# Performance work log

Measured on AMD Instinct MI355X. Metric: run time of the kernel, lower is better.

The kernel has to match this reference:

```python
import jax, jax.numpy as jnp
import numpy as np

B, D_IN, D_OUT = 131072, 256, 256

def setup_inputs() -> dict:
    key = jax.random.key(0)
    k1, k2, k3 = jax.random.split(key, 3)
    x = jax.random.normal(k1, (B, D_IN), dtype=jnp.float32)
    # One weight row / bias scalar per SingleNeuron, concatenated: [D_OUT, D_IN], [D_OUT]
    bound = 1.0 / np.sqrt(D_IN)  # nn.Linear default init scale
    W = jax.random.uniform(k2, (D_OUT, D_IN), dtype=jnp.float32, minval=-bound, maxval=bound)
    b = jax.random.uniform(k3, (D_OUT,), dtype=jnp.float32, minval=-bound, maxval=bound)
    return {"x": x, "W": W, "b": b}

def reference(x, W, b):
    # Fused equivalent of looping per-neuron Linear(in,1), stack(dim=1), squeeze, relu
    return jax.nn.relu(jnp.einsum('bi,oi->bo', x, W) + b)
```

## Files before the change

### kernel.cpp

```cpp
#include <hip/hip_runtime.h>


typedef __attribute__((ext_vector_type(16))) float f32x16;
typedef __attribute__((ext_vector_type(8))) __bf16 bf16x8;

#define MFMA(a, b, c) \
    (c) = __builtin_amdgcn_mfma_f32_32x32x16_bf16((a), (b), (c), 0, 0, 0)

__device__ __forceinline__ void cvt8(const float4& A, const float4& B,
                                     bf16x8& hi, bf16x8& lo) {
    const float f[8] = {A.x, A.y, A.z, A.w, B.x, B.y, B.z, B.w};
#pragma unroll
    for (int j = 0; j < 8; ++j) {
        const unsigned int u = __builtin_bit_cast(unsigned int, f[j]);
        hi[j] = __builtin_bit_cast(__bf16, (unsigned short)(u >> 16));
        const float hf = __builtin_bit_cast(float, u & 0xffff0000u);
        const float lf = f[j] - hf;
        lo[j] = __builtin_bit_cast(__bf16,
                    (unsigned short)(__builtin_bit_cast(unsigned int, lf) >> 16));
    }
}

__device__ __forceinline__ void gload16(const float* g, float* l) {
    __builtin_amdgcn_global_load_lds(
        (const __attribute__((address_space(1))) void*)g,
        (__attribute__((address_space(3))) void*)l, 16, 0, 0);
}

__global__ __launch_bounds__(256)
void wprep_kernel(const float* __restrict__ W,
                  __bf16* __restrict__ whi, __bf16* __restrict__ wlo) {
    const int wv = (int)blockIdx.x * 4 + (threadIdx.x >> 6);
    const int l  = threadIdx.x & 63;
    const int t  = wv & 15;
    const int F  = wv >> 4;
    const int n  = F * 32 + (l & 31);
    const int k  = t * 16 + (l >> 5) * 8;
    const float4 A = *(const float4*)(W + n * 256 + k);
    const float4 B = *(const float4*)(W + n * 256 + k + 4);
    bf16x8 hi, lo;
    cvt8(A, B, hi, lo);
    *(bf16x8*)(whi + wv * 512 + l * 8) = hi;
    *(bf16x8*)(wlo + wv * 512 + l * 8) = lo;
}

__global__ __launch_bounds__(512, 3)
void gemm_mfma_kernel(const float* __restrict__ x,
                      const __bf16* __restrict__ whi,
                      const __bf16* __restrict__ wlo,
                      const float* __restrict__ bias,
                      float* __restrict__ out) {
    __shared__ float xs[3][4096];

    const int tid  = threadIdx.x;
    const int lane = tid & 63;
    const int wid  = tid >> 6;
    const int wm   = wid >> 2;
    const int wn   = wid & 3;

    const int bid = (int)blockIdx.x;
    const int rt  = (bid & 7) * 128 + (bid >> 3);

    const int r31 = lane & 31;
    const int g   = lane >> 5;
    const long row0 = (long)rt * 128;

    const int m0 = wm * 64 + r31;
    const int m1 = m0 + 32;
    const int sw = r31 & 7;

    f32x16 acc[2][2];
#pragma unroll
    for (int i = 0; i < 2; ++i)
#pragma unroll
        for (int j = 0; j < 2; ++j)
#pragma unroll
            for (int r = 0; r < 16; ++r) acc[i][j][r] = 0.f;

    const int fbase0 = (wn * 2) * 16;
    const __bf16* whip = whi + (long)lane * 8;
    const __bf16* wlop = wlo + (long)lane * 8;

    auto STAGE = [&](int b, int chunk) {
#pragma unroll
        for (int j = 0; j < 2; ++j) {
            const int G = j * 512 + tid;
            const int m = G >> 3;
            const int cs = (G & 7) ^ (m & 7);
            const float* gp = x + (row0 + m) * 256 + chunk * 32 + cs * 4;
            float* lp = &xs[b][(j * 512 + wid * 64) * 4];
            gload16(gp, lp);
        }
    };

    auto TSTEP = [&](const float* xb, int t,
                     const bf16x8& bh0, const bf16x8& bl0,
                     const bf16x8& bh1, const bf16x8& bl1) {
        const int c0 = t * 4 + g * 2;
        const float4 A0a = *(const float4*)(xb + m0 * 32 + ((c0 ^ sw) * 4));
        const float4 A0b = *(const float4*)(xb + m0 * 32 + (((c0 + 1) ^ sw) * 4));
        const float4 A1a = *(const float4*)(xb + m1 * 32 + ((c0 ^ sw) * 4));
        const float4 A1b = *(const float4*)(xb + m1 * 32 + (((c0 + 1) ^ sw) * 4));
        bf16x8 ah0, al0, ah1, al1;
        cvt8(A0a, A0b, ah0, al0);
        cvt8(A1a, A1b, ah1, al1);
        MFMA(ah0, bh0, acc[0][0]); MFMA(ah0, bh1, acc[0][1]);
        MFMA(ah1, bh0, acc[1][0]); MFMA(ah1, bh1, acc[1][1]);
        MFMA(ah0, bl0, acc[0][0]); MFMA(ah0, bl1, acc[0][1]);
        MFMA(ah1, bl0, acc[1][0]); MFMA(ah1, bl1, acc[1][1]);
        MFMA(al0, bh0, acc[0][0]); MFMA(al0, bh1, acc[0][1]);
        MFMA(al1, bh0, acc[1][0]); MFMA(al1, bh1, acc[1][1]);
    };

#define CHUNK(c, VM)                                                          \
    {                                                                         \
        asm volatile("s_waitcnt vmcnt(" VM ")" ::: "memory");                 \
        __builtin_amdgcn_s_barrier();                                         \
        const long f0 = (long)(fbase0 + (c) * 2) * 512;                       \
        const long f1 = f0 + 16 * 512;                                        \
        const long h0 = (long)(fbase0 + (c) * 2 + 1) * 512;                   \
        const long h1 = h0 + 16 * 512;                                        \
        const bf16x8 B0h0 = *(const bf16x8*)(whip + f0);                      \
        const bf16x8 B0l0 = *(const bf16x8*)(wlop + f0);                      \
        const bf16x8 B0h1 = *(const bf16x8*)(whip + f1);                      \
        const bf16x8 B0l1 = *(const bf16x8*)(wlop + f1);                      \
        const bf16x8 B1h0 = *(const bf16x8*)(whip + h0);                      \
        const bf16x8 B1l0 = *(const bf16x8*)(wlop + h0);                      \
        const bf16x8 B1h1 = *(const bf16x8*)(whip + h1);                      \
        const bf16x8 B1l1 = *(const bf16x8*)(wlop + h1);                      \
        __builtin_amdgcn_sched_barrier(0);                                    \
        if ((c) + 2 < 8) STAGE(((c) + 2) % 3, (c) + 2);                       \
        const float* xb = &xs[(c) % 3][0];                                    \
        TSTEP(xb, 0, B0h0, B0l0, B0h1, B0l1);                                 \
        TSTEP(xb, 1, B1h0, B1l0, B1h1, B1l1);                                 \
    }

    STAGE(0, 0);
    STAGE(1, 1);
    CHUNK(0, "2")
    CHUNK(1, "2")
    CHUNK(2, "2")
    CHUNK(3, "2")
    CHUNK(4, "2")
    CHUNK(5, "2")
    CHUNK(6, "2")
    CHUNK(7, "0")
#undef CHUNK

    const int  ocol0 = wn * 64;
    const long orow0 = row0 + wm * 64;
    const float bj0 = bias[ocol0 + r31];
    const float bj1 = bias[ocol0 + 32 + r31];

#pragma unroll
    for (int i = 0; i < 2; ++i) {
#pragma unroll
        for (int r = 0; r < 16; ++r) {
            const int rowf = (r & 3) + 8 * (r >> 2) + 4 * g;
            const long row = orow0 + i * 32 + rowf;
            float v0 = acc[i][0][r] + bj0;
            float v1 = acc[i][1][r] + bj1;
            v0 = v0 > 0.f ? v0 : 0.f;
            v1 = v1 > 0.f ? v1 : 0.f;
            out[row * 256 + ocol0 + r31]      = v0;
            out[row * 256 + ocol0 + 32 + r31] = v1;
        }
    }
}

extern "C" void kernel_launch(void* const* d_in, const int* in_sizes, int n_in,
                              void* d_out, int out_size, void* d_ws, size_t ws_size,
                              hipStream_t stream) {
    (void)n_in; (void)ws_size; (void)out_size;
    const float* x = (const float*)d_in[0];
    const float* W = (const float*)d_in[1];
    const float* b = (const float*)d_in[2];
    float* out = (float*)d_out;

    __bf16* whi = (__bf16*)d_ws;
    __bf16* wlo = whi + 65536;

    wprep_kernel<<<32, 256, 0, stream>>>(W, whi, wlo);

    const int M = in_sizes[0] / 256;
    const int grid = M / 128;
    gemm_mfma_kernel<<<grid, 512, 0, stream>>>(x, whi, wlo, b, out);
}
```

Baseline: 263.6 us.

## Halve row tile to 64 per block and raise occupancy to four blocks

```diff
diff --git a/kernel.cpp b/kernel.cpp
--- a/kernel.cpp
+++ b/kernel.cpp
@@ -44,13 +44,13 @@
     *(bf16x8*)(wlo + wv * 512 + l * 8) = lo;
 }
 
-__global__ __launch_bounds__(512, 3)
+__global__ __launch_bounds__(512, 4)
 void gemm_mfma_kernel(const float* __restrict__ x,
                       const __bf16* __restrict__ whi,
                       const __bf16* __restrict__ wlo,
                       const float* __restrict__ bias,
                       float* __restrict__ out) {
-    __shared__ float xs[3][4096];
+    __shared__ float xs[3][2048];
 
     const int tid  = threadIdx.x;
     const int lane = tid & 63;
@@ -59,112 +59,88 @@
     const int wn   = wid & 3;
 
     const int bid = (int)blockIdx.x;
-    const int rt  = (bid & 7) * 128 + (bid >> 3);
+    const int rt  = (bid & 7) * 256 + (bid >> 3);
 
     const int r31 = lane & 31;
     const int g   = lane >> 5;
-    const long row0 = (long)rt * 128;
+    const long row0 = (long)rt * 64;
 
-    const int m0 = wm * 64 + r31;
-    const int m1 = m0 + 32;
+    const int m0 = wm * 32 + r31;
     const int sw = r31 & 7;
 
-    f32x16 acc[2][2];
+    f32x16 acc0, acc1;
 #pragma unroll
-    for (int i = 0; i < 2; ++i)
-#pragma unroll
-        for (int j = 0; j < 2; ++j)
-#pragma unroll
-            for (int r = 0; r < 16; ++r) acc[i][j][r] = 0.f;
+    for (int r = 0; r < 16; ++r) { acc0[r] = 0.f; acc1[r] = 0.f; }
 
     const int fbase0 = (wn * 2) * 16;
     const __bf16* whip = whi + (long)lane * 8;
     const __bf16* wlop = wlo + (long)lane * 8;
 
     auto STAGE = [&](int b, int chunk) {
-#pragma unroll
-        for (int j = 0; j < 2; ++j) {
-            const int G = j * 512 + tid;
-            const int m = G >> 3;
-            const int cs = (G & 7) ^ (m & 7);
-            const float* gp = x + (row0 + m) * 256 + chunk * 32 + cs * 4;
-            float* lp = &xs[b][(j * 512 + wid * 64) * 4];
-            gload16(gp, lp);
-        }
+        const int m = tid >> 3;
+        const int cs = (tid & 7) ^ (m & 7);
+        const float* gp = x + (row0 + m) * 256 + chunk * 32 + cs * 4;
+        float* lp = &xs[b][(wid * 64) * 4];
+        gload16(gp, lp);
     };
 
-    auto TSTEP = [&](const float* xb, int t,
-                     const bf16x8& bh0, const bf16x8& bl0,
-                     const bf16x8& bh1, const bf16x8& bl1) {
+    auto TSTEP = [&](const float* xb, int ks, int t) {
         const int c0 = t * 4 + g * 2;
-        const float4 A0a = *(const float4*)(xb + m0 * 32 + ((c0 ^ sw) * 4));
-        const float4 A0b = *(const float4*)(xb + m0 * 32 + (((c0 + 1) ^ sw) * 4));
-        const float4 A1a = *(const float4*)(xb + m1 * 32 + ((c0 ^ sw) * 4));
-        const float4 A1b = *(const float4*)(xb + m1 * 32 + (((c0 + 1) ^ sw) * 4));
-        bf16x8 ah0, al0, ah1, al1;
-        cvt8(A0a, A0b, ah0, al0);
-        cvt8(A1a, A1b, ah1, al1);
-        MFMA(ah0, bh0, acc[0][0]); MFMA(ah0, bh1, acc[0][1]);
-        MFMA(ah1, bh0, acc[1][0]); MFMA(ah1, bh1, acc[1][1]);
-        MFMA(ah0, bl0, acc[0][0]); MFMA(ah0, bl1, acc[0][1]);
-        MFMA(ah1, bl0, acc[1][0]); MFMA(ah1, bl1, acc[1][1]);
-        MFMA(al0, bh0, acc[0][0]); MFMA(al0, bh1, acc[0][1]);
-        MFMA(al1, bh0, acc[1][0]); MFMA(al1, bh1, acc[1][1]);
+        const float4 Aa = *(const float4*)(xb + m0 * 32 + ((c0 ^ sw) * 4));
+        const float4 Ab = *(const float4*)(xb + m0 * 32 + (((c0 + 1) ^ sw) * 4));
+        bf16x8 ah, al;
+        cvt8(Aa, Ab, ah, al);
+        const long f0 = (long)(fbase0 + ks) * 512;
+        const long f1 = f0 + 16 * 512;
+        {
+            const bf16x8 bh = *(const bf16x8*)(whip + f0);
+            const bf16x8 bl = *(const bf16x8*)(wlop + f0);
+            MFMA(ah, bh, acc0); MFMA(ah, bl, acc0); MFMA(al, bh, acc0);
+        }
+        {
+            const bf16x8 bh = *(const bf16x8*)(whip + f1);
+            const bf16x8 bl = *(const bf16x8*)(wlop + f1);
+            MFMA(ah, bh, acc1); MFMA(ah, bl, acc1); MFMA(al, bh, acc1);
+        }
     };
 
 #define CHUNK(c, VM)                                                          \
     {                                                                         \
         asm volatile("s_waitcnt vmcnt(" VM ")" ::: "memory");                 \
         __builtin_amdgcn_s_barrier();                                         \
-        const long f0 = (long)(fbase0 + (c) * 2) * 512;                       \
-        const long f1 = f0 + 16 * 512;                                        \
-        const long h0 = (long)(fbase0 + (c) * 2 + 1) * 512;                   \
-        const long h1 = h0 + 16 * 512;                                        \
-        const bf16x8 B0h0 = *(const bf16x8*)(whip + f0);                      \
-        const bf16x8 B0l0 = *(const bf16x8*)(wlop + f0);                      \
-        const bf16x8 B0h1 = *(const bf16x8*)(whip + f1);                      \
-        const bf16x8 B0l1 = *(const bf16x8*)(wlop + f1);                      \
-        const bf16x8 B1h0 = *(const bf16x8*)(whip + h0);                      \
-        const bf16x8 B1l0 = *(const bf16x8*)(wlop + h0);                      \
-        const bf16x8 B1h1 = *(const bf16x8*)(whip + h1);                      \
-        const bf16x8 B1l1 = *(const bf16x8*)(wlop + h1);                      \
-        __builtin_amdgcn_sched_barrier(0);                                    \
         if ((c) + 2 < 8) STAGE(((c) + 2) % 3, (c) + 2);                       \
         const float* xb = &xs[(c) % 3][0];                                    \
-        TSTEP(xb, 0, B0h0, B0l0, B0h1, B0l1);                                 \
-        TSTEP(xb, 1, B1h0, B1l0, B1h1, B1l1);                                 \
+        TSTEP(xb, (c) * 2, 0);                                                \
+        TSTEP(xb, (c) * 2 + 1, 1);                                            \
     }
 
     STAGE(0, 0);
     STAGE(1, 1);
-    CHUNK(0, "2")
-    CHUNK(1, "2")
-    CHUNK(2, "2")
-    CHUNK(3, "2")
-    CHUNK(4, "2")
-    CHUNK(5, "2")
-    CHUNK(6, "2")
+    CHUNK(0, "1")
+    CHUNK(1, "1")
+    CHUNK(2, "1")
+    CHUNK(3, "1")
+    CHUNK(4, "1")
+    CHUNK(5, "1")
+    CHUNK(6, "1")
     CHUNK(7, "0")
 #undef CHUNK
 
     const int  ocol0 = wn * 64;
-    const long orow0 = row0 + wm * 64;
+    const long orow0 = row0 + wm * 32;
     const float bj0 = bias[ocol0 + r31];
     const float bj1 = bias[ocol0 + 32 + r31];
 
 #pragma unroll
-    for (int i = 0; i < 2; ++i) {
-#pragma unroll
-        for (int r = 0; r < 16; ++r) {
-            const int rowf = (r & 3) + 8 * (r >> 2) + 4 * g;
-            const long row = orow0 + i * 32 + rowf;
-            float v0 = acc[i][0][r] + bj0;
-            float v1 = acc[i][1][r] + bj1;
-            v0 = v0 > 0.f ? v0 : 0.f;
-            v1 = v1 > 0.f ? v1 : 0.f;
-            out[row * 256 + ocol0 + r31]      = v0;
-            out[row * 256 + ocol0 + 32 + r31] = v1;
-        }
+    for (int r = 0; r < 16; ++r) {
+        const int rowf = (r & 3) + 8 * (r >> 2) + 4 * g;
+        const long row = orow0 + rowf;
+        float v0 = acc0[r] + bj0;
+        float v1 = acc1[r] + bj1;
+        v0 = v0 > 0.f ? v0 : 0.f;
+        v1 = v1 > 0.f ? v1 : 0.f;
+        out[row * 256 + ocol0 + r31]      = v0;
+        out[row * 256 + ocol0 + 32 + r31] = v1;
     }
 }
 
@@ -183,6 +159,6 @@
     wprep_kernel<<<32, 256, 0, stream>>>(W, whi, wlo);
 
     const int M = in_sizes[0] / 256;
-    const int grid = M / 128;
+    const int grid = M / 64;
     gemm_mfma_kernel<<<grid, 512, 0, stream>>>(x, whi, wlo, b, out);
 }
```

New measurement: 272.4 us. 1.03x slower.
